# Kernel optimization log

Measured on AMD Instinct MI355X. Metric: run time of the kernel, lower is better.

## Reference

```python
import jax, jax.numpy as jnp
import numpy as np

D = 2048; H = 16; KV = 4; HD = D // H  # head_dim=128
EPS = 1e-6; THETA = 10000.0


def _rmsnorm(x, w):
    # x: [..., HD]
    var = jnp.mean(x * x, axis=-1, keepdims=True)
    return x * jax.lax.rsqrt(var + EPS) * w


def _rope(x, cos, sin):
    # x: [B, L, nH, HD]; cos/sin: [L, HD//2]; interleaved-pair rotation
    xe = x[..., 0::2]
    xo = x[..., 1::2]
    c = cos[None, :, None, :]
    s = sin[None, :, None, :]
    re = xe * c - xo * s
    ro = xe * s + xo * c
    return jnp.stack([re, ro], axis=-1).reshape(x.shape)


def setup_inputs() -> dict:
    key = jax.random.key(0)
    ks = jax.random.split(key, 8)
    B, L = 2, 2048
    x = jax.random.normal(ks[0], (B, L, D), dtype=jnp.float32)
    wq = jax.random.normal(ks[1], (D, D), dtype=jnp.float32) * 0.02
    wk = jax.random.normal(ks[2], (KV * HD, D), dtype=jnp.float32) * 0.02
    wv = jax.random.normal(ks[3], (KV * HD, D), dtype=jnp.float32) * 0.02
    wo = jax.random.normal(ks[4], (D, D), dtype=jnp.float32) * 0.02
    q_norm_w = jnp.ones((HD,), dtype=jnp.float32)
    k_norm_w = jnp.ones((HD,), dtype=jnp.float32)
    return {"x": x, "wq": wq, "wk": wk, "wv": wv, "wo": wo,
            "q_norm_w": q_norm_w, "k_norm_w": k_norm_w}


def reference(x, wq, wk, wv, wo, q_norm_w, k_norm_w):
    B, L, _ = x.shape
    G = H // KV  # GQA group size (repeat factor)

    q = (x @ wq.T).reshape(B, L, H, HD)
    k = (x @ wk.T).reshape(B, L, KV, HD)
    v = (x @ wv.T).reshape(B, L, KV, HD)

    q = _rmsnorm(q, q_norm_w)
    k = _rmsnorm(k, k_norm_w)

    # RoPE (positions 0..L-1, prompt path)
    inv_freq = 1.0 / (THETA ** (jnp.arange(0, HD, 2, dtype=jnp.float32) / HD))
    ang = jnp.arange(L, dtype=jnp.float32)[:, None] * inv_freq[None, :]  # [L, HD/2]
    cos, sin = jnp.cos(ang), jnp.sin(ang)
    q = _rope(q, cos, sin)
    k = _rope(k, cos, sin)

    # GQA: q head h attends kv head h // G (== repeat_interleave of k,v)
    qg = q.reshape(B, L, KV, G, HD)
    scale = 1.0 / jnp.sqrt(jnp.float32(HD))
    scores = jnp.einsum('bqkgd,bskd->bkgqs', qg, k) * scale  # [B,KV,G,L,L]

    causal = jnp.tril(jnp.ones((L, L), dtype=bool))
    scores = jnp.where(causal, scores, jnp.finfo(scores.dtype).min)
    p = jax.nn.softmax(scores, axis=-1)

    o = jnp.einsum('bkgqs,bskd->bqkgd', p, v).reshape(B, L, D)
    return o @ wo.T
```

## Files before the change

kernel.cpp:

```cpp
#include <hip/hip_runtime.h>
#include <hip/hip_bf16.h>
#include <stdint.h>
#include <stddef.h>

#define D_DIM 2048
#define H_HEADS 16
#define KV_HEADS 4
#define HEAD_DIM 128
#define SEQ_L 2048
#define BATCH 2
#define NTOK 4096
#define NQK 2560
#define NQKV 3072

typedef __attribute__((ext_vector_type(4))) float f32x4;
typedef __attribute__((ext_vector_type(16))) float f32x16;
typedef __attribute__((ext_vector_type(8))) short bf16x8;

__device__ __forceinline__ unsigned short f2bf(float f) {
  __hip_bfloat16 h = __float2bfloat16(f);
  return *reinterpret_cast<unsigned short*>(&h);
}
__device__ __forceinline__ unsigned pack2(float lo, float hi) {
  return (unsigned)f2bf(lo) | ((unsigned)f2bf(hi) << 16);
}
__device__ __forceinline__ float bf2f(unsigned int s) {
  return __uint_as_float(s << 16);
}
__device__ __forceinline__ void plane32swap(unsigned& a, unsigned& b) {
  asm volatile("v_permlane32_swap_b32 %0, %1" : "+v"(a), "+v"(b));
}

__device__ __forceinline__ void async_copy16(const void* g, void* l) {
  __builtin_amdgcn_global_load_lds(
      (__attribute__((address_space(1))) void*)(g),
      (__attribute__((address_space(3))) void*)(l),
      16, 0, 0);
}

__device__ __forceinline__ void cast_seg(const float* __restrict__ src,
                                         unsigned short* __restrict__ dst,
                                         int n4, int gid, int stride) {
  for (int i = gid; i < n4; i += stride) {
    float4 v = *reinterpret_cast<const float4*>(src + (size_t)i * 4);
    uint2 o;
    o.x = pack2(v.x, v.y);
    o.y = pack2(v.z, v.w);
    *reinterpret_cast<uint2*>(dst + (size_t)i * 4) = o;
  }
}

__global__ __launch_bounds__(256) void fused_cast_kernel(
    const float* __restrict__ s0, const float* __restrict__ s1,
    const float* __restrict__ s2, const float* __restrict__ s3,
    const float* __restrict__ s4,
    unsigned short* __restrict__ d0, unsigned short* __restrict__ d1,
    unsigned short* __restrict__ d2, unsigned short* __restrict__ d3,
    unsigned short* __restrict__ d4) {
  int gid = blockIdx.x * blockDim.x + threadIdx.x;
  const int stride = 512 * 256;
  const size_t xh = (size_t)NTOK * D_DIM / 2;
  switch (blockIdx.y) {
    case 0: cast_seg(s0, d0, (NTOK * D_DIM) / 8, gid, stride); break;
    case 1: cast_seg(s0 + xh, d0 + xh, (NTOK * D_DIM) / 8, gid, stride); break;
    case 2: cast_seg(s1, d1, (D_DIM * D_DIM) / 4, gid, stride); break;
    case 3: cast_seg(s4, d4, (D_DIM * D_DIM) / 4, gid, stride); break;
    default:
      cast_seg(s2, d2, (512 * D_DIM) / 4, gid, stride);
      cast_seg(s3, d3, (512 * D_DIM) / 4, gid, stride);
  }
}

__global__ __launch_bounds__(256) void rope_table_kernel(float* __restrict__ cosT,
                                                         float* __restrict__ sinT) {
  int i = blockIdx.x * blockDim.x + threadIdx.x;
  if (i >= SEQ_L * 64) return;
  int p = i & 63;
  float l = (float)(i >> 6);
  float inv = powf(10000.0f, -(float)p / 64.0f);
  float ang = l * inv;
  cosT[i] = cosf(ang);
  sinT[i] = sinf(ang);
}

__device__ __forceinline__ void store_out(unsigned short* p, float v) { *p = f2bf(v); }
__device__ __forceinline__ void store_out(float* p, float v) { *p = v; }

template <typename OutT, bool VSPLIT>
__global__ __launch_bounds__(256) void gemm_bt_kernel(const unsigned short* __restrict__ A,
                                                      const unsigned short* __restrict__ B,
                                                      OutT* __restrict__ C,
                                                      unsigned short* __restrict__ vt,
                                                      int M, int N, int K) {
  __shared__ unsigned short Alds[128 * 32];
  __shared__ unsigned short Blds[128 * 32];
  const int tid = threadIdx.x;
  const int wave = tid >> 6;
  const int lane = tid & 63;
  const int l15 = lane & 15;
  const int l4 = lane >> 4;

  const int nwg = gridDim.x * gridDim.y;
  const int orig = blockIdx.y * gridDim.x + blockIdx.x;
  const int cpx = nwg >> 3;
  const int swz = (orig & 7) * cpx + (orig >> 3);
  const int m0 = (swz % gridDim.x) * 128;
  const int n0 = (swz / gridDim.x) * 128;

  const int wm = (wave >> 1) * 64;
  const int wn = (wave & 1) * 64;

  f32x4 acc[4][4] = {};

  const int soff0 = wave * 1024 + lane * 16;

  for (int kt = 0; kt < K; kt += 32) {
#pragma unroll
    for (int inst = 0; inst < 2; ++inst) {
      int off = soff0 + inst * 4096;
      int row = off >> 6;
      int colb = off & 63;
      const char* ga = (const char*)(A + (size_t)(m0 + row) * K + kt) + colb;
      async_copy16(ga, (char*)Alds + off);
      const char* gb = (const char*)(B + (size_t)(n0 + row) * K + kt) + colb;
      async_copy16(gb, (char*)Blds + off);
    }
    __syncthreads();
    bf16x8 af[4], bfr[4];
#pragma unroll
    for (int i = 0; i < 4; ++i)
      af[i] = *reinterpret_cast<const bf16x8*>(Alds + (wm + i * 16 + l15) * 32 + l4 * 8);
#pragma unroll
    for (int j = 0; j < 4; ++j)
      bfr[j] = *reinterpret_cast<const bf16x8*>(Blds + (wn + j * 16 + l15) * 32 + l4 * 8);
#pragma unroll
    for (int i = 0; i < 4; ++i)
#pragma unroll
      for (int j = 0; j < 4; ++j)
        acc[i][j] = __builtin_amdgcn_mfma_f32_16x16x32_bf16(af[i], bfr[j], acc[i][j], 0, 0, 0);
    __syncthreads();
  }

  if (VSPLIT && n0 >= NQK) {
#pragma unroll
    for (int i = 0; i < 4; ++i)
#pragma unroll
      for (int j = 0; j < 4; ++j) {
        int vrow = n0 + wn + j * 16 + l15 - NQK;
        int tok0 = m0 + wm + i * 16 + l4 * 4;
        ushort4 pk;
        pk.x = f2bf(acc[i][j][0]);
        pk.y = f2bf(acc[i][j][1]);
        pk.z = f2bf(acc[i][j][2]);
        pk.w = f2bf(acc[i][j][3]);
        *reinterpret_cast<ushort4*>(vt + (size_t)vrow * NTOK + tok0) = pk;
      }
    return;
  }

  const int cstride = VSPLIT ? NQK : N;
#pragma unroll
  for (int i = 0; i < 4; ++i)
#pragma unroll
    for (int j = 0; j < 4; ++j) {
      int col = n0 + wn + j * 16 + l15;
#pragma unroll
      for (int r = 0; r < 4; ++r) {
        int row = m0 + wm + i * 16 + l4 * 4 + r;
        store_out(C + (size_t)row * cstride + col, acc[i][j][r]);
      }
    }
}

__global__ __launch_bounds__(256) void norm_rope_kernel(unsigned short* __restrict__ qk,
                                                        const float* __restrict__ qw,
                                                        const float* __restrict__ kw,
                                                        const float* __restrict__ cosT,
                                                        const float* __restrict__ sinT) {
  int gw = (blockIdx.x * blockDim.x + threadIdx.x) >> 6;
  int lane = threadIdx.x & 63;
  int half = lane >> 5;
  int L = lane & 31;
  int rho = gw * 2 + half;
  unsigned short* rowp;
  const float* w;
  int m;
  float sc;
  if (rho < NTOK * H_HEADS) {
    m = rho >> 4;
    rowp = qk + (size_t)m * NQK + (rho & 15) * HEAD_DIM;
    w = qw;
    sc = 0.08838834764831845f;
  } else {
    int r2 = rho - NTOK * H_HEADS;
    m = r2 >> 2;
    rowp = qk + (size_t)m * NQK + D_DIM + (r2 & 3) * HEAD_DIM;
    w = kw;
    sc = 1.0f;
  }
  int l = m & (SEQ_L - 1);
  uint2 pr = *reinterpret_cast<const uint2*>(rowp + L * 4);
  float e0 = bf2f(pr.x & 0xffffu), o0 = bf2f(pr.x >> 16);
  float e1 = bf2f(pr.y & 0xffffu), o1 = bf2f(pr.y >> 16);
  float ss = e0 * e0 + o0 * o0 + e1 * e1 + o1 * o1;
#pragma unroll
  for (int off = 1; off < 32; off <<= 1) ss += __shfl_xor(ss, off);
  float rsn = rsqrtf(ss * (1.0f / 128.0f) + 1e-6f) * sc;
  float4 wv4 = *reinterpret_cast<const float4*>(w + L * 4);
  float2 c2 = *reinterpret_cast<const float2*>(cosT + l * 64 + L * 2);
  float2 s2 = *reinterpret_cast<const float2*>(sinT + l * 64 + L * 2);
  float xe0 = e0 * rsn * wv4.x, xo0 = o0 * rsn * wv4.y;
  float xe1 = e1 * rsn * wv4.z, xo1 = o1 * rsn * wv4.w;
  uint2 outp;
  outp.x = pack2(xe0 * c2.x - xo0 * s2.x, xe0 * s2.x + xo0 * c2.x);
  outp.y = pack2(xe1 * c2.y - xo1 * s2.y, xe1 * s2.y + xo1 * c2.y);
  *reinterpret_cast<uint2*>(rowp + L * 4) = outp;
}

__global__ __launch_bounds__(256, 3) void attn_kernel(const unsigned short* __restrict__ qk,
                                                      const unsigned short* __restrict__ vt,
                                                      unsigned short* __restrict__ obuf,
                                                      unsigned short* __restrict__ p2,
                                                      float* __restrict__ m1G, float* __restrict__ l1G,
                                                      float* __restrict__ m2G, float* __restrict__ l2G) {
  __shared__ unsigned short Kl[64 * 128];
  __shared__ unsigned short Vl[2][128 * 64];
  __shared__ float invl[128];

  const int tid = threadIdx.x;
  const int w = tid >> 6, lane = tid & 63;
  const int l31 = lane & 31, hi = lane >> 5;

  const int jx = blockIdx.x;
  int qt, seg, kv_begin, kv_end;
  bool split;
  if (jx < 16) {
    split = true;
    qt = 15 - (jx >> 1);
    seg = jx & 1;
    int nt = qt + 1;
    kv_begin = seg * nt;
    kv_end = kv_begin + nt;
  } else {
    split = false;
    seg = 0;
    qt = 23 - jx;
    kv_begin = 0;
    kv_end = 2 * qt + 2;
  }
  const int q0 = qt * 128;

  const int bh = blockIdx.y;
  const int b = bh >> 4, h = bh & 15, kvh = h >> 2;

  const unsigned short* Qg = qk + (size_t)(b * SEQ_L + q0 + w * 32 + l31) * NQK + h * HEAD_DIM;
  const unsigned short* Kg = qk + (size_t)(b * SEQ_L) * NQK + D_DIM + kvh * HEAD_DIM;
  const unsigned short* Vg = vt + (size_t)(kvh * HEAD_DIM) * NTOK + b * SEQ_L;

  bf16x8 qf[8];
#pragma unroll
  for (int kk = 0; kk < 8; ++kk)
    qf[kk] = *reinterpret_cast<const bf16x8*>(Qg + kk * 16 + hi * 8);

  f32x16 accO[4] = {};
  float m_run = -1e30f, l_run = 0.0f;

  const int qmin_w = q0 + w * 32;
  const int qmax_w = qmin_w + 31;
  const int qg = qmin_w + l31;

  auto stageK = [&](int kt) {
#pragma unroll
    for (int i = 0; i < 4; ++i) {
      int o = (i * 256 + tid) * 16;
      int row = o >> 8;
      int scb = (o & 255) ^ ((row & 7) << 4);
      const char* src = (const char*)(Kg + (size_t)(kt * 64 + row) * NQK) + scb;
      async_copy16(src, (char*)Kl + o);
    }
  };
  auto stageV = [&](int vb, int kt) {
#pragma unroll
    for (int i = 0; i < 4; ++i) {
      int o = (i * 256 + tid) * 16;
      int d = o >> 7;
      int skb = (o & 127) ^ ((d & 7) << 4);
      const char* src = (const char*)(Vg + (size_t)d * NTOK + kt * 64) + skb;
      async_copy16(src, (char*)(&Vl[vb][0]) + o);
    }
  };

  stageK(kv_begin);
  stageV(0, kv_begin);
  asm volatile("s_waitcnt vmcnt(0)" ::: "memory");
  __syncthreads();

  int vb = 0;
  for (int kt = kv_begin; kt < kv_end; ++kt) {
    const bool active = (kt * 64 <= qmax_w);
    bf16x8 pa[2][2];

    if (active) {
      f32x16 st[2] = {};
      __builtin_amdgcn_s_setprio(1);
#pragma unroll
      for (int stile = 0; stile < 2; ++stile) {
#pragma unroll
        for (int kk = 0; kk < 8; ++kk) {
          int row = stile * 32 + l31;
          int off = (row << 8) + (((kk << 5) + (hi << 4)) ^ ((l31 & 7) << 4));
          bf16x8 kf = *reinterpret_cast<const bf16x8*>((const char*)Kl + off);
          st[stile] = __builtin_amdgcn_mfma_f32_32x32x16_bf16(kf, qf[kk], st[stile], 0, 0, 0);
        }
      }
      __builtin_amdgcn_s_setprio(0);

      const bool need_mask = (kt * 64 + 63 > qmin_w);
      float tmax = -1e30f;
#pragma unroll
      for (int stile = 0; stile < 2; ++stile)
#pragma unroll
        for (int r = 0; r < 16; ++r) {
          float s = st[stile][r];
          if (need_mask) {
            int key = kt * 64 + stile * 32 + (r & 3) + ((r >> 2) << 3) + (hi << 2);
            if (key > qg) s = -1e30f;
          }
          st[stile][r] = s;
          tmax = fmaxf(tmax, s);
        }
      tmax = fmaxf(tmax, __shfl_xor(tmax, 32));

      if (!__all(tmax - m_run <= 8.0f)) {
        float mnew = fmaxf(m_run, tmax);
        float corr = __expf(m_run - mnew);
        m_run = mnew;
        l_run *= corr;
        float corrq[16];
#pragma unroll
        for (int r = 0; r < 16; ++r) {
          int qi = (r & 3) + ((r >> 2) << 3) + (hi << 2);
          corrq[r] = __shfl(corr, qi);
        }
#pragma unroll
        for (int dt = 0; dt < 4; ++dt)
#pragma unroll
          for (int r = 0; r < 16; ++r) accO[dt][r] *= corrq[r];
      }

      float rsum = 0.0f;
#pragma unroll
      for (int stile = 0; stile < 2; ++stile)
#pragma unroll
        for (int r = 0; r < 16; ++r) {
          float pe = __expf(st[stile][r] - m_run);
          st[stile][r] = pe;
          rsum += pe;
        }
      rsum += __shfl_xor(rsum, 32);
      l_run += rsum;

#pragma unroll
      for (int stile = 0; stile < 2; ++stile)
#pragma unroll
        for (int kc = 0; kc < 2; ++kc) {
          int rb = kc * 8;
          unsigned a  = pack2(st[stile][rb + 0], st[stile][rb + 1]);
          unsigned bw = pack2(st[stile][rb + 4], st[stile][rb + 5]);
          unsigned c  = pack2(st[stile][rb + 2], st[stile][rb + 3]);
          unsigned d  = pack2(st[stile][rb + 6], st[stile][rb + 7]);
          plane32swap(a, bw);
          plane32swap(c, d);
          union { bf16x8 v; unsigned u[4]; } uu;
          uu.u[0] = a; uu.u[1] = c; uu.u[2] = bw; uu.u[3] = d;
          pa[stile][kc] = uu.v;
        }
    }

    if (kt + 1 < kv_end) stageV(vb ^ 1, kt + 1);

    __syncthreads();

    if (kt + 1 < kv_end) stageK(kt + 1);

    if (active) {
      __builtin_amdgcn_s_setprio(1);
#pragma unroll
      for (int dt = 0; dt < 4; ++dt) {
        int drow = dt * 32 + l31;
#pragma unroll
        for (int stile = 0; stile < 2; ++stile)
#pragma unroll
          for (int kc = 0; kc < 2; ++kc) {
            int off = (drow << 7) + (((stile << 6) + (kc << 5) + (hi << 4)) ^ ((l31 & 7) << 4));
            bf16x8 vf = *reinterpret_cast<const bf16x8*>((const char*)(&Vl[vb][0]) + off);
            accO[dt] = __builtin_amdgcn_mfma_f32_32x32x16_bf16(pa[stile][kc], vf, accO[dt], 0, 0, 0);
          }
      }
      __builtin_amdgcn_s_setprio(0);
    }

    asm volatile("s_waitcnt vmcnt(0)" ::: "memory");
    __syncthreads();
    vb ^= 1;
  }

  if (!split) {
    if (hi == 0) invl[w * 32 + l31] = 1.0f / l_run;
    __syncthreads();
#pragma unroll
    for (int dt = 0; dt < 4; ++dt)
#pragma unroll
      for (int r = 0; r < 16; ++r) {
        int qrow = (r & 3) + ((r >> 2) << 3) + (hi << 2);
        float val = accO[dt][r] * invl[w * 32 + qrow];
        int tok = b * SEQ_L + q0 + w * 32 + qrow;
        obuf[(size_t)tok * D_DIM + h * HEAD_DIM + dt * 32 + l31] = f2bf(val);
      }
  } else {
    const int rowbase = bh * 1024 + (qt - 8) * 128;
    if (hi == 0) {
      int rr = rowbase + w * 32 + l31;
      if (seg == 0) { m1G[rr] = m_run; l1G[rr] = l_run; }
      else          { m2G[rr] = m_run; l2G[rr] = l_run; }
    }
#pragma unroll
    for (int dt = 0; dt < 4; ++dt)
#pragma unroll
      for (int r = 0; r < 16; ++r) {
        int qrow = (r & 3) + ((r >> 2) << 3) + (hi << 2);
        float val = accO[dt][r];
        if (seg == 0) {
          int tok = b * SEQ_L + q0 + w * 32 + qrow;
          obuf[(size_t)tok * D_DIM + h * HEAD_DIM + dt * 32 + l31] = f2bf(val);
        } else {
          size_t prow = (size_t)(rowbase + w * 32 + qrow);
          p2[prow * HEAD_DIM + dt * 32 + l31] = f2bf(val);
        }
      }
  }
}

__global__ __launch_bounds__(256) void combine_kernel(unsigned short* __restrict__ obuf,
                                                      const unsigned short* __restrict__ p2,
                                                      const float* __restrict__ m1G, const float* __restrict__ l1G,
                                                      const float* __restrict__ m2G, const float* __restrict__ l2G) {
  int gid = blockIdx.x * blockDim.x + threadIdx.x;
  int row = gid >> 4;
  int dc = (gid & 15) * 8;
  int bh = row >> 10;
  int rem = row & 1023;
  int qt = 8 + (rem >> 7);
  int rr = rem & 127;
  int b = bh >> 4, h = bh & 15;
  size_t tok = (size_t)(b * SEQ_L + qt * 128 + rr);

  float m1 = m1G[row], l1 = l1G[row], m2 = m2G[row], l2 = l2G[row];
  float mm = fmaxf(m1, m2);
  float w1 = __expf(m1 - mm), w2 = __expf(m2 - mm);
  float inv = 1.0f / (w1 * l1 + w2 * l2);

  unsigned short* op = obuf + tok * D_DIM + h * HEAD_DIM + dc;
  const unsigned short* pp = p2 + (size_t)row * HEAD_DIM + dc;
  ushort4 a0 = *reinterpret_cast<const ushort4*>(op);
  ushort4 a1 = *reinterpret_cast<const ushort4*>(op + 4);
  ushort4 b0 = *reinterpret_cast<const ushort4*>(pp);
  ushort4 b1 = *reinterpret_cast<const ushort4*>(pp + 4);
  ushort4 o0, o1;
  o0.x = f2bf((w1 * bf2f(a0.x) + w2 * bf2f(b0.x)) * inv);
  o0.y = f2bf((w1 * bf2f(a0.y) + w2 * bf2f(b0.y)) * inv);
  o0.z = f2bf((w1 * bf2f(a0.z) + w2 * bf2f(b0.z)) * inv);
  o0.w = f2bf((w1 * bf2f(a0.w) + w2 * bf2f(b0.w)) * inv);
  o1.x = f2bf((w1 * bf2f(a1.x) + w2 * bf2f(b1.x)) * inv);
  o1.y = f2bf((w1 * bf2f(a1.y) + w2 * bf2f(b1.y)) * inv);
  o1.z = f2bf((w1 * bf2f(a1.z) + w2 * bf2f(b1.z)) * inv);
  o1.w = f2bf((w1 * bf2f(a1.w) + w2 * bf2f(b1.w)) * inv);
  *reinterpret_cast<ushort4*>(op) = o0;
  *reinterpret_cast<ushort4*>(op + 4) = o1;
}

extern "C" void kernel_launch(void* const* d_in, const int* in_sizes, int n_in,
                              void* d_out, int out_size, void* d_ws, size_t ws_size,
                              hipStream_t stream) {
  const float* x   = (const float*)d_in[0];
  const float* wq  = (const float*)d_in[1];
  const float* wk  = (const float*)d_in[2];
  const float* wv  = (const float*)d_in[3];
  const float* wo  = (const float*)d_in[4];
  const float* qnw = (const float*)d_in[5];
  const float* knw = (const float*)d_in[6];
  float* out = (float*)d_out;

  char* ws = (char*)d_ws;
  unsigned short* Xb    = (unsigned short*)(ws);
  unsigned short* Wqkvb = (unsigned short*)(ws + 16777216);
  unsigned short* Wob   = (unsigned short*)(ws + 29360128);
  unsigned short* QKb   = (unsigned short*)(ws + 37748736);
  unsigned short* VTb   = (unsigned short*)(ws + 58720256);
  unsigned short* Obuf  = (unsigned short*)(ws + 62914560);
  float* cosT = (float*)(ws + 79691776);
  float* sinT = (float*)(ws + 80216064);

  unsigned short* P2 = (unsigned short*)(ws);
  float* m1G = (float*)(ws + 8388608);
  float* l1G = (float*)(ws + 8519680);
  float* m2G = (float*)(ws + 8650752);
  float* l2G = (float*)(ws + 8781824);

  fused_cast_kernel<<<dim3(512, 5), 256, 0, stream>>>(
      x, wq, wk, wv, wo,
      Xb, Wqkvb,
      Wqkvb + (size_t)D_DIM * D_DIM,
      Wqkvb + (size_t)NQK * D_DIM,
      Wob);
  rope_table_kernel<<<512, 256, 0, stream>>>(cosT, sinT);

  dim3 g1(NTOK / 128, NQKV / 128);
  gemm_bt_kernel<unsigned short, true><<<g1, 256, 0, stream>>>(
      Xb, Wqkvb, QKb, VTb, NTOK, NQKV, D_DIM);

  norm_rope_kernel<<<(NTOK * (H_HEADS + KV_HEADS)) / 8, 256, 0, stream>>>(
      QKb, qnw, knw, cosT, sinT);

  attn_kernel<<<dim3(24, BATCH * H_HEADS), 256, 0, stream>>>(
      QKb, VTb, Obuf, P2, m1G, l1G, m2G, l2G);
  combine_kernel<<<2048, 256, 0, stream>>>(Obuf, P2, m1G, l1G, m2G, l2G);

  dim3 g2(NTOK / 128, D_DIM / 128);
  gemm_bt_kernel<float, false><<<g2, 256, 0, stream>>>(
      Obuf, Wob, out, nullptr, NTOK, D_DIM, D_DIM);
}
```

Before: 239.9 us.

## Single-buffer V tile to raise attention occupancy; fold RoPE table into cast kernel

The attention kernel drops the double-buffered V tile in LDS, cutting shared memory per block so launch bounds can ask for four blocks per CU instead of three. V for the next tile is now loaded after the PV MMAs finish, followed by a full wait and an extra barrier, so V loads no longer overlap with compute. The separate RoPE cos/sin table kernel is merged into the fused cast kernel as a sixth grid row, removing one launch. The bet is that the extra occupancy hides more latency than the lost V prefetch overlap costs.

```diff
diff --git a/kernel.cpp b/kernel.cpp
--- a/kernel.cpp
+++ b/kernel.cpp
@@ -56,7 +56,8 @@
     const float* __restrict__ s4,
     unsigned short* __restrict__ d0, unsigned short* __restrict__ d1,
     unsigned short* __restrict__ d2, unsigned short* __restrict__ d3,
-    unsigned short* __restrict__ d4) {
+    unsigned short* __restrict__ d4,
+    float* __restrict__ cosT, float* __restrict__ sinT) {
   int gid = blockIdx.x * blockDim.x + threadIdx.x;
   const int stride = 512 * 256;
   const size_t xh = (size_t)NTOK * D_DIM / 2;
@@ -65,22 +66,19 @@
     case 1: cast_seg(s0 + xh, d0 + xh, (NTOK * D_DIM) / 8, gid, stride); break;
     case 2: cast_seg(s1, d1, (D_DIM * D_DIM) / 4, gid, stride); break;
     case 3: cast_seg(s4, d4, (D_DIM * D_DIM) / 4, gid, stride); break;
-    default:
+    case 4:
       cast_seg(s2, d2, (512 * D_DIM) / 4, gid, stride);
       cast_seg(s3, d3, (512 * D_DIM) / 4, gid, stride);
-  }
-}
-
-__global__ __launch_bounds__(256) void rope_table_kernel(float* __restrict__ cosT,
-                                                         float* __restrict__ sinT) {
-  int i = blockIdx.x * blockDim.x + threadIdx.x;
-  if (i >= SEQ_L * 64) return;
-  int p = i & 63;
-  float l = (float)(i >> 6);
-  float inv = powf(10000.0f, -(float)p / 64.0f);
-  float ang = l * inv;
-  cosT[i] = cosf(ang);
-  sinT[i] = sinf(ang);
+      break;
+    default: {
+      int p = gid & 63;
+      float l = (float)(gid >> 6);
+      float inv = powf(10000.0f, -(float)p / 64.0f);
+      float ang = l * inv;
+      cosT[gid] = cosf(ang);
+      sinT[gid] = sinf(ang);
+    }
+  }
 }
 
 __device__ __forceinline__ void store_out(unsigned short* p, float v) { *p = f2bf(v); }
@@ -217,14 +215,14 @@
   *reinterpret_cast<uint2*>(rowp + L * 4) = outp;
 }
 
-__global__ __launch_bounds__(256, 3) void attn_kernel(const unsigned short* __restrict__ qk,
+__global__ __launch_bounds__(256, 4) void attn_kernel(const unsigned short* __restrict__ qk,
                                                       const unsigned short* __restrict__ vt,
                                                       unsigned short* __restrict__ obuf,
                                                       unsigned short* __restrict__ p2,
                                                       float* __restrict__ m1G, float* __restrict__ l1G,
                                                       float* __restrict__ m2G, float* __restrict__ l2G) {
   __shared__ unsigned short Kl[64 * 128];
-  __shared__ unsigned short Vl[2][128 * 64];
+  __shared__ unsigned short Vl[128 * 64];
   __shared__ float invl[128];
 
   const int tid = threadIdx.x;
@@ -279,23 +277,22 @@
       async_copy16(src, (char*)Kl + o);
     }
   };
-  auto stageV = [&](int vb, int kt) {
+  auto stageV = [&](int kt) {
 #pragma unroll
     for (int i = 0; i < 4; ++i) {
       int o = (i * 256 + tid) * 16;
       int d = o >> 7;
       int skb = (o & 127) ^ ((d & 7) << 4);
       const char* src = (const char*)(Vg + (size_t)d * NTOK + kt * 64) + skb;
-      async_copy16(src, (char*)(&Vl[vb][0]) + o);
+      async_copy16(src, (char*)Vl + o);
     }
   };
 
   stageK(kv_begin);
-  stageV(0, kv_begin);
+  stageV(kv_begin);
   asm volatile("s_waitcnt vmcnt(0)" ::: "memory");
   __syncthreads();
 
-  int vb = 0;
   for (int kt = kv_begin; kt < kv_end; ++kt) {
     const bool active = (kt * 64 <= qmax_w);
     bf16x8 pa[2][2];
@@ -377,8 +374,6 @@
         }
     }
 
-    if (kt + 1 < kv_end) stageV(vb ^ 1, kt + 1);
-
     __syncthreads();
 
     if (kt + 1 < kv_end) stageK(kt + 1);
@@ -393,16 +388,20 @@
 #pragma unroll
           for (int kc = 0; kc < 2; ++kc) {
             int off = (drow << 7) + (((stile << 6) + (kc << 5) + (hi << 4)) ^ ((l31 & 7) << 4));
-            bf16x8 vf = *reinterpret_cast<const bf16x8*>((const char*)(&Vl[vb][0]) + off);
+            bf16x8 vf = *reinterpret_cast<const bf16x8*>((const char*)Vl + off);
             accO[dt] = __builtin_amdgcn_mfma_f32_32x32x16_bf16(pa[stile][kc], vf, accO[dt], 0, 0, 0);
           }
       }
       __builtin_amdgcn_s_setprio(0);
     }
 
-    asm volatile("s_waitcnt vmcnt(0)" ::: "memory");
     __syncthreads();
-    vb ^= 1;
+
+    if (kt + 1 < kv_end) {
+      stageV(kt + 1);
+      asm volatile("s_waitcnt vmcnt(0)" ::: "memory");
+    }
+    __syncthreads();
   }
 
   if (!split) {
@@ -507,13 +506,12 @@
   float* m2G = (float*)(ws + 8650752);
   float* l2G = (float*)(ws + 8781824);
 
-  fused_cast_kernel<<<dim3(512, 5), 256, 0, stream>>>(
+  fused_cast_kernel<<<dim3(512, 6), 256, 0, stream>>>(
       x, wq, wk, wv, wo,
       Xb, Wqkvb,
       Wqkvb + (size_t)D_DIM * D_DIM,
       Wqkvb + (size_t)NQK * D_DIM,
-      Wob);
-  rope_table_kernel<<<512, 256, 0, stream>>>(cosT, sinT);
+      Wob, cosT, sinT);
 
   dim3 g1(NTOK / 128, NQKV / 128);
   gemm_bt_kernel<unsigned short, true><<<g1, 256, 0, stream>>>(
```

Result: slower. 372.6 us (+55.3%).
